# Kernel tuning notes

Hardware: AMD Instinct MI355X
Metric: run time of the kernel (lower is better)

Reference implementation:

```python
import jax, jax.numpy as jnp
import numpy as np

B, T, D, H = 2, 2048, 1024, 16
HD = D // H  # 64
THETA = 10000.0


def _rope(x, pos):
    # x: (B,H,T,HD), pos: (T,) int
    half = HD // 2
    inv_freq = THETA ** (-jnp.arange(half, dtype=jnp.float32) * 2.0 / HD)  # (half,)
    ang = pos.astype(jnp.float32)[:, None] * inv_freq[None, :]  # (T, half)
    cos = jnp.cos(ang)[None, None]  # (1,1,T,half)
    sin = jnp.sin(ang)[None, None]
    x1 = x[..., 0::2]
    x2 = x[..., 1::2]
    r1 = x1 * cos - x2 * sin
    r2 = x1 * sin + x2 * cos
    return jnp.stack([r1, r2], axis=-1).reshape(x.shape)


def setup_inputs() -> dict:
    key = jax.random.key(0)
    ks = jax.random.split(key, 9)
    s = 0.02
    inp = {
        "x": jax.random.normal(ks[0], (B, T, D), dtype=jnp.float32),
        "token_positions": jnp.arange(T, dtype=jnp.int64),
        "wq": jax.random.normal(ks[1], (D, D), dtype=jnp.float32) * s,
        "bq": jnp.zeros((D,), dtype=jnp.float32),
        "wk": jax.random.normal(ks[2], (D, D), dtype=jnp.float32) * s,
        "bk": jnp.zeros((D,), dtype=jnp.float32),
        "wv": jax.random.normal(ks[3], (D, D), dtype=jnp.float32) * s,
        "bv": jnp.zeros((D,), dtype=jnp.float32),
        "wo": jax.random.normal(ks[4], (D, D), dtype=jnp.float32) * s,
        "bo": jnp.zeros((D,), dtype=jnp.float32),
    }
    return inp


def reference(x, token_positions, wq, bq, wk, bk, wv, bv, wo, bo):
    # Linear projections (torch Linear: x @ W.T + b)
    q = x @ wq.T + bq
    k = x @ wk.T + bk
    v = x @ wv.T + bv
    # (B,T,D) -> (B,H,T,HD)
    q = q.reshape(B, T, H, HD).transpose(0, 2, 1, 3)
    k = k.reshape(B, T, H, HD).transpose(0, 2, 1, 3)
    v = v.reshape(B, T, H, HD).transpose(0, 2, 1, 3)
    # RoPE on q and k
    q = _rope(q, token_positions)
    k = _rope(k, token_positions)
    # causal masked softmax attention
    scores = jnp.einsum('bhqd,bhkd->bhqk', q, k) / jnp.sqrt(jnp.float32(HD))
    keep = jnp.tril(jnp.ones((T, T), dtype=bool))  # keep mask (True = attend)
    scores = jnp.where(keep[None, None], scores, -jnp.inf)
    probs = jax.nn.softmax(scores, axis=-1)
    out = jnp.einsum('bhqk,bhkd->bhqd', probs, v)
    out = out.transpose(0, 2, 1, 3).reshape(B, T, D)
    return out @ wo.T + bo
```

## Files before the change

kernel.cpp:

```cpp
#include <hip/hip_runtime.h>
#include <hip/hip_bf16.h>

#define Bc 2
#define Tc 2048
#define Dc 1024
#define Hc 16
#define HDc 64

typedef __attribute__((ext_vector_type(4))) float f32x4;
typedef __attribute__((ext_vector_type(8))) short short8;
typedef __bf16 bf16x8 __attribute__((ext_vector_type(8)));

static __device__ __forceinline__ short f2bf(float f) {
  union { float f; unsigned u; } v; v.f = f;
  unsigned r = v.u + 0x7fffu + ((v.u >> 16) & 1u);
  return (short)(r >> 16);
}

static __device__ __forceinline__ f32x4 mfma16(bf16x8 a, bf16x8 b, f32x4 c) {
  return __builtin_amdgcn_mfma_f32_16x16x32_bf16(a, b, c, 0, 0, 0);
}

__global__ __launch_bounds__(256) void wconv_kernel(
    const float* __restrict__ wq, const float* __restrict__ wk,
    const float* __restrict__ wv, short* __restrict__ Wb)
{
  const int z = blockIdx.y;
  const float* src = (z == 0) ? wq : (z == 1) ? wk : wv;
  const size_t i = ((size_t)blockIdx.x * 256 + threadIdx.x) * 8;
  const float4 a0 = *(const float4*)(src + i);
  const float4 a1 = *(const float4*)(src + i + 4);
  short8 r;
  r[0] = f2bf(a0.x); r[1] = f2bf(a0.y); r[2] = f2bf(a0.z); r[3] = f2bf(a0.w);
  r[4] = f2bf(a1.x); r[5] = f2bf(a1.y); r[6] = f2bf(a1.z); r[7] = f2bf(a1.w);
  *(short8*)(Wb + (size_t)z * 1048576 + i) = r;
}

__global__ __launch_bounds__(256) void rope_tab_kernel(
    const int* __restrict__ tp, float2* __restrict__ tab)
{
  const int idx = blockIdx.x * 256 + threadIdx.x;
  const int t = idx >> 5, i = idx & 31;
  const float inv = expf((float)i * -0.2878231366242557f);
  float sn, cs;
  sincosf((float)tp[t] * inv, &sn, &cs);
  tab[idx] = make_float2(cs, sn);
}

__global__ __launch_bounds__(256) void qkv_kernel(
    const float* __restrict__ x, const short* __restrict__ Wb,
    const float* __restrict__ bq, const float* __restrict__ bk,
    const float* __restrict__ bv, const float2* __restrict__ rtab,
    short* __restrict__ Qw, short* __restrict__ Kw, short* __restrict__ Vw)
{
  __shared__ short As[64][40];
  __shared__ short Bs[3][64][40];
  const int tid = threadIdx.x, lane = tid & 63, w = tid >> 6;
  const int wr = w >> 1, wc = w & 1;
  const int nbase = blockIdx.x * 64, mbase = blockIdx.y * 64;
  const int srow = tid >> 2, scol = (tid & 3) * 8;
  const int fr = lane & 15, fq = lane >> 4, kg = fq * 8;

  f32x4 acc[3][2][2] = {};

  for (int k0 = 0; k0 < Dc; k0 += 32) {
    if (k0) __syncthreads();
    {
      const float* src = x + (size_t)(mbase + srow) * Dc + k0 + scol;
      const float4 a0 = *(const float4*)src;
      const float4 a1 = *(const float4*)(src + 4);
      short* dst = &As[srow][scol];
      dst[0] = f2bf(a0.x); dst[1] = f2bf(a0.y); dst[2] = f2bf(a0.z); dst[3] = f2bf(a0.w);
      dst[4] = f2bf(a1.x); dst[5] = f2bf(a1.y); dst[6] = f2bf(a1.z); dst[7] = f2bf(a1.w);
    }
#pragma unroll
    for (int z = 0; z < 3; ++z)
      *(short8*)&Bs[z][srow][scol] =
          *(const short8*)(Wb + (size_t)z * 1048576 + (size_t)(nbase + srow) * Dc + k0 + scol);
    __syncthreads();
    const bf16x8 af0 = *(const bf16x8*)&As[wr * 32 + fr][kg];
    const bf16x8 af1 = *(const bf16x8*)&As[wr * 32 + 16 + fr][kg];
#pragma unroll
    for (int z = 0; z < 3; ++z) {
      const bf16x8 b0 = *(const bf16x8*)&Bs[z][wc * 32 + fr][kg];
      const bf16x8 b1 = *(const bf16x8*)&Bs[z][wc * 32 + 16 + fr][kg];
      acc[z][0][0] = mfma16(af0, b0, acc[z][0][0]);
      acc[z][0][1] = mfma16(af0, b1, acc[z][0][1]);
      acc[z][1][0] = mfma16(af1, b0, acc[z][1][0]);
      acc[z][1][1] = mfma16(af1, b1, acc[z][1][1]);
    }
  }

#pragma unroll
  for (int a2 = 0; a2 < 2; ++a2)
#pragma unroll
    for (int b2 = 0; b2 < 2; ++b2) {
      const int n = nbase + wc * 32 + b2 * 16 + fr;
      const float bi0 = bq[n], bi1 = bk[n], bi2 = bv[n];
      const int hd = n & 63, h = n >> 6;
#pragma unroll
      for (int r = 0; r < 4; ++r) {
        const int m = mbase + wr * 32 + a2 * 16 + fq * 4 + r;
        const int t = m & (Tc - 1);
        const int bbi = m >> 11;
        const size_t oidx = (((size_t)bbi * Hc + h) * Tc + t) * HDc + hd;
        const float2 cs = rtab[t * 32 + (hd >> 1)];
        float v0 = acc[0][a2][b2][r] + bi0;
        float v1 = acc[1][a2][b2][r] + bi1;
        const float n0 = __shfl_xor(v0, 1);
        const float n1 = __shfl_xor(v1, 1);
        v0 = (hd & 1) ? (n0 * cs.y + v0 * cs.x) : (v0 * cs.x - n0 * cs.y);
        v1 = (hd & 1) ? (n1 * cs.y + v1 * cs.x) : (v1 * cs.x - n1 * cs.y);
        Qw[oidx] = f2bf(v0);
        Kw[oidx] = f2bf(v1);
        Vw[oidx] = f2bf(acc[2][a2][b2][r] + bi2);
      }
    }
}

__global__ __launch_bounds__(256) void out_kernel(
    const short* __restrict__ Ob, const float* __restrict__ wo,
    const float* __restrict__ bo, float* __restrict__ out)
{
  __shared__ short As[64][40];
  __shared__ short Bs[64][40];
  const int tid = threadIdx.x, lane = tid & 63, w = tid >> 6;
  const int wr = w >> 1, wc = w & 1;
  const int nbase = blockIdx.x * 64, mbase = blockIdx.y * 64;
  const int srow = tid >> 2, scol = (tid & 3) * 8;
  const int fr = lane & 15, fq = lane >> 4, kg = fq * 8;

  f32x4 acc[2][2] = {};

  for (int k0 = 0; k0 < Dc; k0 += 32) {
    if (k0) __syncthreads();
    *(short8*)&As[srow][scol] = *(const short8*)(Ob + (size_t)(mbase + srow) * Dc + k0 + scol);
    {
      const float* src = wo + (size_t)(nbase + srow) * Dc + k0 + scol;
      const float4 b0 = *(const float4*)src;
      const float4 b1 = *(const float4*)(src + 4);
      short* dst = &Bs[srow][scol];
      dst[0] = f2bf(b0.x); dst[1] = f2bf(b0.y); dst[2] = f2bf(b0.z); dst[3] = f2bf(b0.w);
      dst[4] = f2bf(b1.x); dst[5] = f2bf(b1.y); dst[6] = f2bf(b1.z); dst[7] = f2bf(b1.w);
    }
    __syncthreads();
    const bf16x8 af0 = *(const bf16x8*)&As[wr * 32 + fr][kg];
    const bf16x8 af1 = *(const bf16x8*)&As[wr * 32 + 16 + fr][kg];
    const bf16x8 b0 = *(const bf16x8*)&Bs[wc * 32 + fr][kg];
    const bf16x8 b1 = *(const bf16x8*)&Bs[wc * 32 + 16 + fr][kg];
    acc[0][0] = mfma16(af0, b0, acc[0][0]);
    acc[0][1] = mfma16(af0, b1, acc[0][1]);
    acc[1][0] = mfma16(af1, b0, acc[1][0]);
    acc[1][1] = mfma16(af1, b1, acc[1][1]);
  }

#pragma unroll
  for (int a2 = 0; a2 < 2; ++a2)
#pragma unroll
    for (int b2 = 0; b2 < 2; ++b2) {
      const int n = nbase + wc * 32 + b2 * 16 + fr;
      const float bv = bo[n];
#pragma unroll
      for (int r = 0; r < 4; ++r) {
        const int m = mbase + wr * 32 + a2 * 16 + fq * 4 + r;
        out[(size_t)m * Dc + n] = acc[a2][b2][r] + bv;
      }
    }
}

__global__ __launch_bounds__(256) void attn_kernel(
    const short* __restrict__ Qw, const short* __restrict__ Kw,
    const short* __restrict__ Vw, short* __restrict__ Ob)
{
  __shared__ short Ks[64][72];
  __shared__ short Vt[64][72];
  __shared__ short Ps[64][72];
  const int tid = threadIdx.x, lane = tid & 63, w = tid >> 6;
  const int bh = blockIdx.y, bb = bh >> 4, h = bh & 15;
  const int qt = (int)gridDim.x - 1 - blockIdx.x;
  const int q0 = qt * 64;
  const size_t base = (size_t)bh * Tc * HDc;
  const int fr = lane & 15, fq = lane >> 4, kg = fq * 8;

  bf16x8 qf[2];
  {
    const short* qrow = Qw + base + (size_t)(q0 + w * 16 + fr) * HDc;
    qf[0] = *(const bf16x8*)(qrow + kg);
    qf[1] = *(const bf16x8*)(qrow + 32 + kg);
  }

  f32x4 o[4] = {};
  float mrun[4] = {-1e30f, -1e30f, -1e30f, -1e30f};
  float lrun[4] = {0.f, 0.f, 0.f, 0.f};

  const int srow = tid >> 2;
  const int scol = (tid & 3) * 16;

  const int ntiles = qt + 1;
  for (int kt = 0; kt < ntiles; ++kt) {
    const int kv0 = kt * 64;
    __syncthreads();
    {
      const short* ksrc = Kw + base + (size_t)(kv0 + srow) * HDc + scol;
      *(short8*)&Ks[srow][scol] = *(const short8*)ksrc;
      *(short8*)&Ks[srow][scol + 8] = *(const short8*)(ksrc + 8);
      const short* vsrc = Vw + base + (size_t)(kv0 + srow) * HDc + scol;
#pragma unroll
      for (int j = 0; j < 16; ++j) {
        const int row = scol + j;
        Vt[row][(srow + (row & 56)) & 63] = vsrc[j];
      }
    }
    __syncthreads();

    f32x4 s[4];
#pragma unroll
    for (int cf = 0; cf < 4; ++cf) {
      f32x4 acc = {};
      acc = mfma16(qf[0], *(const bf16x8*)&Ks[cf * 16 + fr][kg], acc);
      acc = mfma16(qf[1], *(const bf16x8*)&Ks[cf * 16 + fr][32 + kg], acc);
      s[cf] = acc * 0.125f;
    }
    if (kt == ntiles - 1) {
#pragma unroll
      for (int cf = 0; cf < 4; ++cf) {
        const int col = kv0 + cf * 16 + fr;
#pragma unroll
        for (int r = 0; r < 4; ++r) {
          const int row = q0 + w * 16 + fq * 4 + r;
          if (col > row) s[cf][r] = -1e30f;
        }
      }
    }
    float pm[4];
#pragma unroll
    for (int r = 0; r < 4; ++r)
      pm[r] = fmaxf(fmaxf(s[0][r], s[1][r]), fmaxf(s[2][r], s[3][r]));
#pragma unroll
    for (int d = 1; d < 16; d <<= 1)
#pragma unroll
      for (int r = 0; r < 4; ++r)
        pm[r] = fmaxf(pm[r], __shfl_xor(pm[r], d));
    float alpha[4], rs[4];
#pragma unroll
    for (int r = 0; r < 4; ++r) {
      const float mn = fmaxf(mrun[r], pm[r]);
      alpha[r] = __expf(mrun[r] - mn);
      mrun[r] = mn;
      rs[r] = 0.f;
    }
#pragma unroll
    for (int cf = 0; cf < 4; ++cf)
#pragma unroll
      for (int r = 0; r < 4; ++r) {
        const float p = __expf(s[cf][r] - mrun[r]);
        s[cf][r] = p;
        rs[r] += p;
      }
#pragma unroll
    for (int d = 1; d < 16; d <<= 1)
#pragma unroll
      for (int r = 0; r < 4; ++r)
        rs[r] += __shfl_xor(rs[r], d);
#pragma unroll
    for (int r = 0; r < 4; ++r)
      lrun[r] = lrun[r] * alpha[r] + rs[r];
#pragma unroll
    for (int df = 0; df < 4; ++df)
#pragma unroll
      for (int r = 0; r < 4; ++r)
        o[df][r] *= alpha[r];
    {
      const int rowxor = (4 * w + fq) & 7;
#pragma unroll
      for (int cf = 0; cf < 4; ++cf) {
        const int cblk = 2 * cf + (fr >> 3);
        const int colp = (((cblk ^ rowxor) << 3) + (fr & 7));
#pragma unroll
        for (int r = 0; r < 4; ++r)
          Ps[w * 16 + fq * 4 + r][colp] = f2bf(s[cf][r]);
      }
    }
    __syncthreads();
#pragma unroll
    for (int ks = 0; ks < 2; ++ks) {
      const int prow = w * 16 + fr;
      const bf16x8 pa = *(const bf16x8*)&Ps[prow][((4 * ks + fq) ^ ((prow >> 2) & 7)) << 3];
#pragma unroll
      for (int df = 0; df < 4; ++df) {
        const int vr = df * 16 + fr;
        const bf16x8 vb = *(const bf16x8*)&Vt[vr][(ks * 32 + kg + (vr & 56)) & 63];
        o[df] = mfma16(pa, vb, o[df]);
      }
    }
  }

#pragma unroll
  for (int df = 0; df < 4; ++df)
#pragma unroll
    for (int r = 0; r < 4; ++r) {
      const int t = q0 + w * 16 + fq * 4 + r;
      const float val = o[df][r] / lrun[r];
      Ob[((size_t)bb * Tc + t) * Dc + h * HDc + df * 16 + fr] = f2bf(val);
    }
}

extern "C" void kernel_launch(void* const* d_in, const int* in_sizes, int n_in,
                              void* d_out, int out_size, void* d_ws, size_t ws_size,
                              hipStream_t stream) {
  const float* x  = (const float*)d_in[0];
  const int*   tp = (const int*)d_in[1];
  const float* wq = (const float*)d_in[2];
  const float* bq = (const float*)d_in[3];
  const float* wk = (const float*)d_in[4];
  const float* bk = (const float*)d_in[5];
  const float* wv = (const float*)d_in[6];
  const float* bv = (const float*)d_in[7];
  const float* wo = (const float*)d_in[8];
  const float* bo = (const float*)d_in[9];
  float* out = (float*)d_out;

  char* ws = (char*)d_ws;
  short* Qw = (short*)(ws);
  short* Kw = (short*)(ws + (8u << 20));
  short* Vw = (short*)(ws + (16u << 20));
  short* Ob = (short*)(ws + (24u << 20));
  short*  Wb   = (short*)(ws + (24u << 20));
  float2* rtab = (float2*)(ws + (30u << 20));

  dim3 blk(256);
  wconv_kernel<<<dim3(512, 3), blk, 0, stream>>>(wq, wk, wv, Wb);
  rope_tab_kernel<<<dim3(256), blk, 0, stream>>>(tp, rtab);
  qkv_kernel<<<dim3(16, 64), blk, 0, stream>>>(x, Wb, bq, bk, bv, rtab, Qw, Kw, Vw);
  attn_kernel<<<dim3(32, 32), blk, 0, stream>>>(Qw, Kw, Vw, Ob);
  out_kernel<<<dim3(16, 64), blk, 0, stream>>>(Ob, wo, bo, out);
}
```

Baseline: 310.8 us.

## Store V transposed from QKV and use single-wave attention blocks reading K/V from global

```diff
diff --git a/kernel.cpp b/kernel.cpp
--- a/kernel.cpp
+++ b/kernel.cpp
@@ -8,6 +8,7 @@
 #define HDc 64
 
 typedef __attribute__((ext_vector_type(4))) float f32x4;
+typedef __attribute__((ext_vector_type(4))) short short4v;
 typedef __attribute__((ext_vector_type(8))) short short8;
 typedef __bf16 bf16x8 __attribute__((ext_vector_type(8)));
 
@@ -98,11 +99,13 @@
       const int n = nbase + wc * 32 + b2 * 16 + fr;
       const float bi0 = bq[n], bi1 = bk[n], bi2 = bv[n];
       const int hd = n & 63, h = n >> 6;
+      const int mb = mbase + wr * 32 + a2 * 16 + fq * 4;
+      const int tb = mb & (Tc - 1);
+      const int bbi = mb >> 11;
+      short4v pv;
 #pragma unroll
       for (int r = 0; r < 4; ++r) {
-        const int m = mbase + wr * 32 + a2 * 16 + fq * 4 + r;
-        const int t = m & (Tc - 1);
-        const int bbi = m >> 11;
+        const int t = tb + r;
         const size_t oidx = (((size_t)bbi * Hc + h) * Tc + t) * HDc + hd;
         const float2 cs = rtab[t * 32 + (hd >> 1)];
         float v0 = acc[0][a2][b2][r] + bi0;
@@ -113,8 +116,9 @@
         v1 = (hd & 1) ? (n1 * cs.y + v1 * cs.x) : (v1 * cs.x - n1 * cs.y);
         Qw[oidx] = f2bf(v0);
         Kw[oidx] = f2bf(v1);
-        Vw[oidx] = f2bf(acc[2][a2][b2][r] + bi2);
+        pv[r] = f2bf(acc[2][a2][b2][r] + bi2);
       }
+      *(short4v*)(Vw + ((size_t)(bbi * Hc + h) * HDc + hd) * Tc + tb) = pv;
     }
 }
 
@@ -168,68 +172,56 @@
     }
 }
 
-__global__ __launch_bounds__(256) void attn_kernel(
+__global__ __launch_bounds__(64) void attn_kernel(
     const short* __restrict__ Qw, const short* __restrict__ Kw,
-    const short* __restrict__ Vw, short* __restrict__ Ob)
-{
-  __shared__ short Ks[64][72];
-  __shared__ short Vt[64][72];
-  __shared__ short Ps[64][72];
-  const int tid = threadIdx.x, lane = tid & 63, w = tid >> 6;
+    const short* __restrict__ Vtg, short* __restrict__ Ob)
+{
+  __shared__ short Ps[16][72];
+  const int lane = threadIdx.x;
   const int bh = blockIdx.y, bb = bh >> 4, h = bh & 15;
   const int qt = (int)gridDim.x - 1 - blockIdx.x;
-  const int q0 = qt * 64;
-  const size_t base = (size_t)bh * Tc * HDc;
+  const int q16 = qt * 16;
+  const size_t baseQ = (size_t)bh * Tc * HDc;
+  const size_t baseV = (size_t)bh * HDc * Tc;
   const int fr = lane & 15, fq = lane >> 4, kg = fq * 8;
 
-  bf16x8 qf[2];
+  bf16x8 qf0, qf1;
   {
-    const short* qrow = Qw + base + (size_t)(q0 + w * 16 + fr) * HDc;
-    qf[0] = *(const bf16x8*)(qrow + kg);
-    qf[1] = *(const bf16x8*)(qrow + 32 + kg);
+    const short* qrow = Qw + baseQ + (size_t)(q16 + fr) * HDc;
+    qf0 = *(const bf16x8*)(qrow + kg);
+    qf1 = *(const bf16x8*)(qrow + 32 + kg);
   }
 
   f32x4 o[4] = {};
   float mrun[4] = {-1e30f, -1e30f, -1e30f, -1e30f};
   float lrun[4] = {0.f, 0.f, 0.f, 0.f};
 
-  const int srow = tid >> 2;
-  const int scol = (tid & 3) * 16;
-
-  const int ntiles = qt + 1;
+  const int ntiles = (qt >> 2) + 1;
   for (int kt = 0; kt < ntiles; ++kt) {
     const int kv0 = kt * 64;
-    __syncthreads();
-    {
-      const short* ksrc = Kw + base + (size_t)(kv0 + srow) * HDc + scol;
-      *(short8*)&Ks[srow][scol] = *(const short8*)ksrc;
-      *(short8*)&Ks[srow][scol + 8] = *(const short8*)(ksrc + 8);
-      const short* vsrc = Vw + base + (size_t)(kv0 + srow) * HDc + scol;
-#pragma unroll
-      for (int j = 0; j < 16; ++j) {
-        const int row = scol + j;
-        Vt[row][(srow + (row & 56)) & 63] = vsrc[j];
-      }
-    }
-    __syncthreads();
-
     f32x4 s[4];
 #pragma unroll
     for (int cf = 0; cf < 4; ++cf) {
+      const short* kr = Kw + baseQ + (size_t)(kv0 + cf * 16 + fr) * HDc + kg;
       f32x4 acc = {};
-      acc = mfma16(qf[0], *(const bf16x8*)&Ks[cf * 16 + fr][kg], acc);
-      acc = mfma16(qf[1], *(const bf16x8*)&Ks[cf * 16 + fr][32 + kg], acc);
+      acc = mfma16(qf0, *(const bf16x8*)kr, acc);
+      acc = mfma16(qf1, *(const bf16x8*)(kr + 32), acc);
       s[cf] = acc * 0.125f;
     }
+    bf16x8 vb[2][4];
+#pragma unroll
+    for (int ks = 0; ks < 2; ++ks)
+#pragma unroll
+      for (int df = 0; df < 4; ++df)
+        vb[ks][df] = *(const bf16x8*)(Vtg + baseV + (size_t)(df * 16 + fr) * Tc + kv0 + ks * 32 + kg);
+
     if (kt == ntiles - 1) {
 #pragma unroll
       for (int cf = 0; cf < 4; ++cf) {
         const int col = kv0 + cf * 16 + fr;
 #pragma unroll
-        for (int r = 0; r < 4; ++r) {
-          const int row = q0 + w * 16 + fq * 4 + r;
-          if (col > row) s[cf][r] = -1e30f;
-        }
+        for (int r = 0; r < 4; ++r)
+          if (col > q16 + fq * 4 + r) s[cf][r] = -1e30f;
       }
     }
     float pm[4];
@@ -270,28 +262,17 @@
 #pragma unroll
       for (int r = 0; r < 4; ++r)
         o[df][r] *= alpha[r];
-    {
-      const int rowxor = (4 * w + fq) & 7;
-#pragma unroll
-      for (int cf = 0; cf < 4; ++cf) {
-        const int cblk = 2 * cf + (fr >> 3);
-        const int colp = (((cblk ^ rowxor) << 3) + (fr & 7));
-#pragma unroll
-        for (int r = 0; r < 4; ++r)
-          Ps[w * 16 + fq * 4 + r][colp] = f2bf(s[cf][r]);
-      }
-    }
-    __syncthreads();
+#pragma unroll
+    for (int cf = 0; cf < 4; ++cf)
+#pragma unroll
+      for (int r = 0; r < 4; ++r)
+        Ps[fq * 4 + r][cf * 16 + fr] = f2bf(s[cf][r]);
 #pragma unroll
     for (int ks = 0; ks < 2; ++ks) {
-      const int prow = w * 16 + fr;
-      const bf16x8 pa = *(const bf16x8*)&Ps[prow][((4 * ks + fq) ^ ((prow >> 2) & 7)) << 3];
-#pragma unroll
-      for (int df = 0; df < 4; ++df) {
-        const int vr = df * 16 + fr;
-        const bf16x8 vb = *(const bf16x8*)&Vt[vr][(ks * 32 + kg + (vr & 56)) & 63];
-        o[df] = mfma16(pa, vb, o[df]);
-      }
+      const bf16x8 pa = *(const bf16x8*)&Ps[fr][ks * 32 + kg];
+#pragma unroll
+      for (int df = 0; df < 4; ++df)
+        o[df] = mfma16(pa, vb[ks][df], o[df]);
     }
   }
 
@@ -299,7 +280,7 @@
   for (int df = 0; df < 4; ++df)
 #pragma unroll
     for (int r = 0; r < 4; ++r) {
-      const int t = q0 + w * 16 + fq * 4 + r;
+      const int t = q16 + fq * 4 + r;
       const float val = o[df][r] / lrun[r];
       Ob[((size_t)bb * Tc + t) * Dc + h * HDc + df * 16 + fr] = f2bf(val);
     }
@@ -332,6 +313,6 @@
   wconv_kernel<<<dim3(512, 3), blk, 0, stream>>>(wq, wk, wv, Wb);
   rope_tab_kernel<<<dim3(256), blk, 0, stream>>>(tp, rtab);
   qkv_kernel<<<dim3(16, 64), blk, 0, stream>>>(x, Wb, bq, bk, bv, rtab, Qw, Kw, Vw);
-  attn_kernel<<<dim3(32, 32), blk, 0, stream>>>(Qw, Kw, Vw, Ob);
+  attn_kernel<<<dim3(128, 32), dim3(64), 0, stream>>>(Qw, Kw, Vw, Ob);
   out_kernel<<<dim3(16, 64), blk, 0, stream>>>(Ob, wo, bo, out);
 }
```

Measured after the change: 339.0 us. +9.1%, slower.
